# Kernel optimization log

Measured on AMD Instinct MI355X. Metric: run time of the kernel, lower is better.

The kernel has to match this reference:

```python
import jax, jax.numpy as jnp
import numpy as np

N_ENT = 15000
N_REL = 237
HID = 128
N_STEP = 3
EPS = 1e-10
E_BASE = 200000
BATCH, NEG = 8, 16


def _lstm(x, w_ih, w_hh, b_ih, b_hh):
    # x: [T, B, H]; single-layer PyTorch-style LSTM (gate order i, f, g, o)
    B = x.shape[1]
    H = w_hh.shape[1]
    bias = b_ih + b_hh

    def step(carry, xt):
        h, c = carry
        gates = xt @ w_ih.T + h @ w_hh.T + bias  # [B, 4H]
        i, f, g, o = jnp.split(gates, 4, axis=-1)
        c = jax.nn.sigmoid(f) * c + jax.nn.sigmoid(i) * jnp.tanh(g)
        h = jax.nn.sigmoid(o) * jnp.tanh(c)
        return (h, c), h

    init = (jnp.zeros((B, H), x.dtype), jnp.zeros((B, H), x.dtype))
    _, hs = jax.lax.scan(step, init, x)
    return hs  # [T, B, H]


def setup_inputs() -> dict:
    key = jax.random.key(0)
    ks = jax.random.split(key, 16)
    h_index = jax.random.randint(ks[0], (BATCH, NEG), 0, N_ENT)
    t_index = jax.random.randint(ks[1], (BATCH, NEG), 0, N_ENT)
    r_index = jax.random.randint(ks[2], (BATCH, NEG), 0, N_REL)
    src = jax.random.randint(ks[3], (E_BASE,), 0, N_ENT)
    dst = jax.random.randint(ks[4], (E_BASE,), 0, N_ENT)
    rel = jax.random.randint(ks[5], (E_BASE,), 0, N_REL)
    edge_weight = jnp.ones((2 * E_BASE,), jnp.float32)
    s = 0.05
    query_emb = jax.random.normal(ks[6], (2 * N_REL + 1, HID), jnp.float32) * s
    w_ih = jax.random.normal(ks[7], (4 * HID, HID), jnp.float32) * s
    w_hh = jax.random.normal(ks[8], (4 * HID, HID), jnp.float32) * s
    b_ih = jax.random.normal(ks[9], (4 * HID,), jnp.float32) * s
    b_hh = jax.random.normal(ks[10], (4 * HID,), jnp.float32) * s
    weight_w = jax.random.normal(ks[11], (2 * N_REL, HID), jnp.float32) * s
    weight_b = jax.random.normal(ks[12], (2 * N_REL,), jnp.float32) * s
    lin_w = jax.random.normal(ks[13], (), jnp.float32)
    lin_b = jax.random.normal(ks[14], (), jnp.float32)
    return {"query_emb": query_emb, "w_ih": w_ih, "w_hh": w_hh, "b_ih": b_ih,
            "b_hh": b_hh, "weight_w": weight_w, "weight_b": weight_b,
            "lin_w": lin_w, "lin_b": lin_b, "edge_weight": edge_weight,
            "h_index": h_index, "t_index": t_index, "r_index": r_index,
            "src": src, "dst": dst, "rel": rel}


def reference(query_emb, w_ih, w_hh, b_ih, b_hh, weight_w, weight_b,
              lin_w, lin_b, edge_weight, h_index, t_index, r_index,
              src, dst, rel):
    R2 = 2 * N_REL
    # graph.undirected(add_inverse=True): add reversed edges with inverse relations
    node_in = jnp.concatenate([src, dst])
    node_out = jnp.concatenate([dst, src])
    relation = jnp.concatenate([rel, rel + N_REL])

    # negative_sample_to_tail
    is_t_neg = jnp.all(h_index == h_index[:, :1], axis=-1, keepdims=True)
    h_i = jnp.where(is_t_neg, h_index, t_index)
    t_i = jnp.where(is_t_neg, t_index, h_index)
    r_i = jnp.where(is_t_neg, r_index, r_index + N_REL)

    hr = (h_i * R2 + r_i).ravel()
    uniq, inv = jnp.unique(hr, return_inverse=True, size=hr.shape[0], fill_value=0)
    inv = inv.ravel().reshape(h_i.shape)
    h_set = uniq // R2
    r_set = uniq % R2
    B = uniq.shape[0]

    # query sequence: [r]*(T-1) + [end=R2]
    q_idx = jnp.concatenate([jnp.tile(r_set[None], (N_STEP - 1, 1)),
                             jnp.full((1, B), R2, r_set.dtype)], axis=0)
    query = query_emb[q_idx]                      # [T, B, H]
    hidden = _lstm(query, w_ih, w_hh, b_ih, b_hh)  # [T, B, H]

    memory = jax.nn.one_hot(h_set, N_ENT, dtype=query.dtype)[None]  # [1, B, N]
    out = None
    for i in range(N_STEP):
        k = hidden[i]                                   # [B, H]
        attn = jax.nn.softmax(jnp.einsum('bd,tbd->bt', k, hidden[:i + 1]), axis=-1)
        inp = jnp.einsum('bt,tbn->nb', attn, memory)    # [N, B]
        w = jax.nn.softmax(k @ weight_w.T + weight_b, axis=-1).T  # [R2, B]
        # gather -> relation-weight multiply -> scatter_add
        msg = inp[node_in] * w[relation] * edge_weight[:, None]   # [2E, B]
        out = jnp.zeros((N_ENT, B), inp.dtype).at[node_out].add(msg)
        out = out / jnp.maximum(out.sum(axis=0, keepdims=True), EPS)
        memory = jnp.concatenate([memory, out.T[None]], axis=0)

    score = out[t_i, inv]          # [batch, neg]
    return score * lin_w + lin_b
```

## Files before the change

### kernel.cpp

```cpp
#include <hip/hip_runtime.h>
#include <math.h>

#define N_ENT  15000
#define N_RELC 237
#define R2C    474
#define EBASE  200000
#define E2     400000
#define EPSV   1e-10f
#define CAP    72
#define NSLICE 64

typedef unsigned int uint32;
typedef unsigned short ushort16;

__device__ __forceinline__ ushort16 f2bf(float x) {
    uint32 u = __float_as_uint(x);
    u = (u + 0x7FFFu + ((u >> 16) & 1u)) >> 16;
    return (ushort16)u;
}
__device__ __forceinline__ float bflo(uint32 u) { return __uint_as_float(u << 16); }
__device__ __forceinline__ float bfhi(uint32 u) { return __uint_as_float(u & 0xFFFF0000u); }

__global__ void init_kernel(float* __restrict__ out0, int* __restrict__ cursor,
                            float* __restrict__ Swide,
                            const float* __restrict__ w_ih, const float* __restrict__ w_hh,
                            const float* __restrict__ weight_w,
                            float* __restrict__ wit, float* __restrict__ wht,
                            float* __restrict__ wwt,
                            const int* __restrict__ h_index, const int* __restrict__ t_index,
                            const int* __restrict__ r_index,
                            int* __restrict__ h_set, int* __restrict__ r_set,
                            int* __restrict__ invp, int* __restrict__ t_flat,
                            int* __restrict__ headidx) {
    if (blockIdx.x == gridDim.x - 1) {
        __shared__ int sv[128], eq[128], f_[128], uniq[128], hsh[128];
        __shared__ int isneg[8];
        __shared__ int UcntS;
        int j = threadIdx.x;
        for (int idx = j; idx < N_ENT; idx += 256) headidx[idx] = -1;
        __syncthreads();
        int hrv = 0, first = 0, rank = 0;
        if (j < 128) {
            int b = j >> 4;
            int h = h_index[j];
            eq[j] = (h == h_index[b * 16]) ? 1 : 0;
        }
        __syncthreads();
        if (j < 128 && (j & 15) == 0) {
            int b = j >> 4, a = 1;
            for (int q = 0; q < 16; q++) a &= eq[b * 16 + q];
            isneg[b] = a;
        }
        __syncthreads();
        if (j < 128) {
            int b = j >> 4;
            int h = h_index[j], t = t_index[j], r = r_index[j];
            int hi, ti, ri;
            if (isneg[b]) { hi = h; ti = t; ri = r; }
            else          { hi = t; ti = h; ri = r + N_RELC; }
            t_flat[j] = ti;
            hrv = hi * R2C + ri;
            sv[j] = hrv;
            uniq[j] = 0;
        }
        __syncthreads();
        if (j < 128) {
            first = 1;
            for (int q = 0; q < j; q++) if (sv[q] == hrv) { first = 0; break; }
            f_[j] = first;
        }
        __syncthreads();
        if (j < 128) {
            for (int q = 0; q < 128; q++) rank += (f_[q] && sv[q] < hrv) ? 1 : 0;
        }
        if (j == 0) {
            int c = 0;
            for (int q = 0; q < 128; q++) c += f_[q];
            UcntS = c;
        }
        __syncthreads();
        if (j < 128) {
            if (first) uniq[rank] = hrv;
            invp[j] = rank;
        }
        __syncthreads();
        if (j < 128) {
            int uv = uniq[j];
            int hs = uv / R2C;
            h_set[j] = hs;
            r_set[j] = uv % R2C;
            hsh[j] = hs;
        }
        __syncthreads();
        if (j < 128) {
            int U = UcntS;
            int hs = hsh[j];
            if (j < U && (j == 0 || hsh[j - 1] != hs)) {
                int e = j + 1;
                while (e < U && hsh[e] == hs) e++;
                headidx[hs] = (j << 8) | e;
            }
        }
        return;
    }
    int idx = blockIdx.x * 256 + threadIdx.x;
    float4 z4 = make_float4(0.f, 0.f, 0.f, 0.f);
    if (idx < 480000) { ((float4*)out0)[idx] = z4; return; }
    idx -= 480000;
    if (idx < 3750) { ((int4*)cursor)[idx] = make_int4(0, 0, 0, 0); return; }
    idx -= 3750;
    if (idx < 6144) { ((float4*)Swide)[idx] = z4; return; }
    idx -= 6144;
    if (idx < 65536) {
        int d = idx >> 9, g = idx & 511;
        wit[idx] = w_ih[g * 128 + d];
        wht[idx] = w_hh[g * 128 + d];
        return;
    }
    idx -= 65536;
    if (idx < 65536) {
        int d = idx >> 9, r = idx & 511;
        if (r < R2C) wwt[idx] = weight_w[r * 128 + d];
    }
}

__global__ void fill_kernel(const int* __restrict__ src, const int* __restrict__ dst,
                            const int* __restrict__ rel, const float* __restrict__ ew,
                            int* __restrict__ cursor, int2* __restrict__ edata2) {
    int e = blockIdx.x * 256 + threadIdx.x;
    if (e >= E2) return;
    int ni, no, r;
    if (e < EBASE) { ni = src[e]; no = dst[e]; r = rel[e]; }
    else { int e2 = e - EBASE; ni = dst[e2]; no = src[e2]; r = rel[e2] + N_RELC; }
    int pos = atomicAdd(&cursor[no], 1);
    if (pos < CAP)
        edata2[no * CAP + pos] = make_int2((ni << 9) | r, __float_as_int(ew[e]));
}

__global__ void lstm_kernel(const float* __restrict__ query_emb,
                            const int* __restrict__ r_set,
                            const float* __restrict__ wit, const float* __restrict__ wht,
                            const float* __restrict__ b_ih, const float* __restrict__ b_hh,
                            float* __restrict__ hidden) {
    int b = blockIdx.x, g = threadIdx.x;
    __shared__ float x[128], h[128], gl[512];
    float bias = b_ih[g] + b_hh[g];
    if (g < 128) x[g] = query_emb[r_set[b] * 128 + g];
    __syncthreads();
    float p0 = 0.f, p1 = 0.f, p2 = 0.f, p3 = 0.f;
    #pragma unroll 8
    for (int d = 0; d < 128; d += 4) {
        p0 += x[d + 0] * wit[(d + 0) * 512 + g];
        p1 += x[d + 1] * wit[(d + 1) * 512 + g];
        p2 += x[d + 2] * wit[(d + 2) * 512 + g];
        p3 += x[d + 3] * wit[(d + 3) * 512 + g];
    }
    float xpA = bias + ((p0 + p1) + (p2 + p3));
    __syncthreads();
    if (g < 128) x[g] = query_emb[R2C * 128 + g];
    __syncthreads();
    p0 = p1 = p2 = p3 = 0.f;
    #pragma unroll 8
    for (int d = 0; d < 128; d += 4) {
        p0 += x[d + 0] * wit[(d + 0) * 512 + g];
        p1 += x[d + 1] * wit[(d + 1) * 512 + g];
        p2 += x[d + 2] * wit[(d + 2) * 512 + g];
        p3 += x[d + 3] * wit[(d + 3) * 512 + g];
    }
    float xpB = bias + ((p0 + p1) + (p2 + p3));
    if (g < 128) h[g] = 0.f;
    float c = 0.f;
    __syncthreads();
    for (int step = 0; step < 3; step++) {
        float a0 = 0.f, a1 = 0.f, a2 = 0.f, a3 = 0.f;
        #pragma unroll 8
        for (int d = 0; d < 128; d += 4) {
            a0 += h[d + 0] * wht[(d + 0) * 512 + g];
            a1 += h[d + 1] * wht[(d + 1) * 512 + g];
            a2 += h[d + 2] * wht[(d + 2) * 512 + g];
            a3 += h[d + 3] * wht[(d + 3) * 512 + g];
        }
        gl[g] = ((step < 2) ? xpA : xpB) + ((a0 + a1) + (a2 + a3));
        __syncthreads();
        if (g < 128) {
            float ig = gl[g], fg = gl[128 + g], gg = gl[256 + g], og = gl[384 + g];
            float si = 1.f / (1.f + expf(-ig));
            float sf = 1.f / (1.f + expf(-fg));
            float so = 1.f / (1.f + expf(-og));
            c = sf * c + si * tanhf(gg);
            float hh = so * tanhf(c);
            hidden[(step * 128 + b) * 128 + g] = hh;
            h[g] = hh;
        }
        __syncthreads();
    }
}

__global__ void coef_kernel(const float* __restrict__ hidden, int step,
                            const float* __restrict__ Swide,
                            const float* __restrict__ wwt,
                            const float* __restrict__ weight_b,
                            ushort16* __restrict__ wTb, float* __restrict__ attnS) {
    int b = blockIdx.x, tid = threadIdx.x;
    __shared__ float k[128];
    __shared__ float red[256];
    __shared__ float sc[3];
    __shared__ float Ssum[2];
    __shared__ float logit[R2C];
    if (tid < 128) k[tid] = hidden[(step * 128 + b) * 128 + tid];
    __syncthreads();
    for (int t = 0; t <= step; t++) {
        float v = 0.f;
        if (tid < 128) v = k[tid] * hidden[(t * 128 + b) * 128 + tid];
        red[tid] = v;
        __syncthreads();
        for (int s2 = 128; s2 > 0; s2 >>= 1) {
            if (tid < s2) red[tid] += red[tid + s2];
            __syncthreads();
        }
        if (tid == 0) sc[t] = red[0];
        __syncthreads();
    }
    for (int t = 0; t < step; t++) {
        red[tid] = (tid < NSLICE) ? Swide[t * (NSLICE * 128) + tid * 128 + b] : 0.f;
        __syncthreads();
        for (int s2 = 128; s2 > 0; s2 >>= 1) {
            if (tid < s2) red[tid] += red[tid + s2];
            __syncthreads();
        }
        if (tid == 0) Ssum[t] = red[0];
        __syncthreads();
    }
    if (tid == 0) {
        float m = sc[0];
        for (int t2 = 1; t2 <= step; t2++) m = fmaxf(m, sc[t2]);
        float ssum = 0.f;
        float ex[3];
        for (int t2 = 0; t2 <= step; t2++) { ex[t2] = expf(sc[t2] - m); ssum += ex[t2]; }
        for (int t2 = 0; t2 <= step; t2++) {
            float a = ex[t2] / ssum;
            if (t2 > 0) a /= fmaxf(Ssum[t2 - 1], EPSV);
            attnS[b * 4 + t2] = a;
        }
    }
    for (int r = tid; r < R2C; r += 256) {
        float acc = weight_b[r];
        #pragma unroll 8
        for (int d = 0; d < 128; d++) acc += k[d] * wwt[d * 512 + r];
        logit[r] = acc;
    }
    __syncthreads();
    float m = -1e30f;
    for (int r = tid; r < R2C; r += 256) m = fmaxf(m, logit[r]);
    red[tid] = m; __syncthreads();
    for (int s2 = 128; s2 > 0; s2 >>= 1) {
        if (tid < s2) red[tid] = fmaxf(red[tid], red[tid + s2]);
        __syncthreads();
    }
    m = red[0]; __syncthreads();
    float s = 0.f;
    for (int r = tid; r < R2C; r += 256) s += expf(logit[r] - m);
    red[tid] = s; __syncthreads();
    for (int s2 = 128; s2 > 0; s2 >>= 1) {
        if (tid < s2) red[tid] += red[tid + s2];
        __syncthreads();
    }
    float invs = 1.f / red[0];
    for (int r = tid; r < R2C; r += 256)
        wTb[r * 128 + b] = f2bf(expf(logit[r] - m) * invs);
}

__global__ void step0_kernel(const int* __restrict__ src, const int* __restrict__ dst,
                             const int* __restrict__ rel, const float* __restrict__ ew,
                             const int* __restrict__ headidx,
                             const ushort16* __restrict__ wTb,
                             float* __restrict__ out0, float* __restrict__ Sw0) {
    int e = blockIdx.x * 256 + threadIdx.x;
    if (e >= E2) return;
    int ni, no, r;
    if (e < EBASE) { ni = src[e]; no = dst[e]; r = rel[e]; }
    else { int e2 = e - EBASE; ni = dst[e2]; no = src[e2]; r = rel[e2] + N_RELC; }
    int hv = headidx[ni];
    if (hv < 0) return;
    float w = ew[e];
    int b0 = hv >> 8, b1 = hv & 255;
    int sl = (e & (NSLICE - 1)) * 128;
    for (int b = b0; b < b1; b++) {
        float v = __uint_as_float(((uint32)wTb[r * 128 + b]) << 16) * w;
        atomicAdd(&out0[no * 128 + b], v);
        atomicAdd(&Sw0[sl + b], v);
    }
}

__global__ void inp_kernel(const float* __restrict__ o1, const float* __restrict__ o2,
                           int step, const float* __restrict__ attnS,
                           const int* __restrict__ h_set, ushort16* __restrict__ inpb) {
    int b = threadIdx.x;
    float a0 = attnS[b * 4 + 0];
    float a1 = attnS[b * 4 + 1];
    float a2 = (step >= 2) ? attnS[b * 4 + 2] : 0.f;
    int hs = h_set[b];
    for (int n = blockIdx.x; n < N_ENT; n += gridDim.x) {
        float v = (n == hs) ? a0 : 0.f;
        v += a1 * o1[n * 128 + b];
        if (step >= 2) v += a2 * o2[n * 128 + b];
        inpb[n * 128 + b] = f2bf(v);
    }
}

__global__ void gather_kernel(const int2* __restrict__ edata2,
                              const int* __restrict__ cursor,
                              const ushort16* __restrict__ inpb,
                              const ushort16* __restrict__ wTb,
                              float* __restrict__ out, float* __restrict__ Sw) {
    __shared__ float sred[4][128];
    int wid = threadIdx.x >> 6;
    int lane = threadIdx.x & 63;
    int n = blockIdx.x * 4 + wid;
    int deg = cursor[n];
    if (deg > CAP) deg = CAP;
    const int2* ed = edata2 + n * CAP;
    int c2 = lane * 2;
    float ax = 0.f, ay = 0.f;
    int e = 0;
    for (; e + 4 <= deg; e += 4) {
        int2 d0 = ed[e + 0], d1 = ed[e + 1], d2 = ed[e + 2], d3 = ed[e + 3];
        uint32 i0 = *(const uint32*)(inpb + ((d0.x >> 9) << 7) + c2);
        uint32 w0 = *(const uint32*)(wTb  + ((d0.x & 511) << 7) + c2);
        uint32 i1 = *(const uint32*)(inpb + ((d1.x >> 9) << 7) + c2);
        uint32 w1 = *(const uint32*)(wTb  + ((d1.x & 511) << 7) + c2);
        uint32 i2 = *(const uint32*)(inpb + ((d2.x >> 9) << 7) + c2);
        uint32 w2 = *(const uint32*)(wTb  + ((d2.x & 511) << 7) + c2);
        uint32 i3 = *(const uint32*)(inpb + ((d3.x >> 9) << 7) + c2);
        uint32 w3 = *(const uint32*)(wTb  + ((d3.x & 511) << 7) + c2);
        float f0 = __int_as_float(d0.y), f1 = __int_as_float(d1.y);
        float f2 = __int_as_float(d2.y), f3 = __int_as_float(d3.y);
        ax += bflo(i0) * bflo(w0) * f0 + bflo(i1) * bflo(w1) * f1
            + bflo(i2) * bflo(w2) * f2 + bflo(i3) * bflo(w3) * f3;
        ay += bfhi(i0) * bfhi(w0) * f0 + bfhi(i1) * bfhi(w1) * f1
            + bfhi(i2) * bfhi(w2) * f2 + bfhi(i3) * bfhi(w3) * f3;
    }
    for (; e < deg; e++) {
        int2 edv = ed[e];
        float w = __int_as_float(edv.y);
        uint32 ia = *(const uint32*)(inpb + ((edv.x >> 9) << 7) + c2);
        uint32 wa = *(const uint32*)(wTb  + ((edv.x & 511) << 7) + c2);
        ax += bflo(ia) * bflo(wa) * w;
        ay += bfhi(ia) * bfhi(wa) * w;
    }
    *(float2*)(out + n * 128 + c2) = make_float2(ax, ay);
    sred[wid][c2] = ax;
    sred[wid][c2 + 1] = ay;
    __syncthreads();
    if (threadIdx.x < 128) {
        float s = sred[0][threadIdx.x] + sred[1][threadIdx.x]
                + sred[2][threadIdx.x] + sred[3][threadIdx.x];
        atomicAdd(&Sw[(blockIdx.x & (NSLICE - 1)) * 128 + threadIdx.x], s);
    }
}

__global__ void score_kernel(const float* __restrict__ out2, const float* __restrict__ Swide,
                             const int* __restrict__ t_flat, const int* __restrict__ invp,
                             const float* __restrict__ lin_w, const float* __restrict__ lin_b,
                             float* __restrict__ d_out) {
    int j = threadIdx.x;
    int bb = invp[j];
    float s = 0.f;
    for (int s8 = 0; s8 < NSLICE; s8++)
        s += Swide[2 * (NSLICE * 128) + s8 * 128 + bb];
    d_out[j] = out2[t_flat[j] * 128 + bb] / fmaxf(s, EPSV) * lin_w[0] + lin_b[0];
}

extern "C" void kernel_launch(void* const* d_in, const int* in_sizes, int n_in,
                              void* d_out, int out_size, void* d_ws, size_t ws_size,
                              hipStream_t stream) {
    const float* query_emb  = (const float*)d_in[0];
    const float* w_ih       = (const float*)d_in[1];
    const float* w_hh       = (const float*)d_in[2];
    const float* b_ih       = (const float*)d_in[3];
    const float* b_hh       = (const float*)d_in[4];
    const float* weight_w   = (const float*)d_in[5];
    const float* weight_b   = (const float*)d_in[6];
    const float* lin_w      = (const float*)d_in[7];
    const float* lin_b      = (const float*)d_in[8];
    const float* edge_weight= (const float*)d_in[9];
    const int*   h_index    = (const int*)d_in[10];
    const int*   t_index    = (const int*)d_in[11];
    const int*   r_index    = (const int*)d_in[12];
    const int*   src        = (const int*)d_in[13];
    const int*   dst        = (const int*)d_in[14];
    const int*   rel        = (const int*)d_in[15];
    float* out = (float*)d_out;

    char* ws = (char*)d_ws;
    size_t off_b = 0;
    auto alloc = [&](size_t bytes) -> void* {
        void* p = ws + off_b;
        off_b = (off_b + bytes + 255) & ~(size_t)255;
        return p;
    };
    float*    hidden  = (float*)alloc(3 * 128 * 128 * sizeof(float));
    float*    attnS   = (float*)alloc(128 * 4 * sizeof(float));
    ushort16* wTb     = (ushort16*)alloc(R2C * 128 * sizeof(ushort16));
    float*    Swide   = (float*)alloc(3 * NSLICE * 128 * sizeof(float));
    float*    wit     = (float*)alloc(512 * 128 * sizeof(float));
    float*    wht     = (float*)alloc(512 * 128 * sizeof(float));
    float*    wwt     = (float*)alloc(512 * 128 * sizeof(float));
    int*      h_set   = (int*)alloc(128 * sizeof(int));
    int*      r_set   = (int*)alloc(128 * sizeof(int));
    int*      invp    = (int*)alloc(128 * sizeof(int));
    int*      t_flat  = (int*)alloc(128 * sizeof(int));
    int*      cursor  = (int*)alloc(N_ENT * sizeof(int));
    int*      headidx = (int*)alloc(N_ENT * sizeof(int));
    int2*     edata2  = (int2*)alloc((size_t)N_ENT * CAP * sizeof(int2));
    ushort16* inpb    = (ushort16*)alloc((size_t)N_ENT * 128 * sizeof(ushort16));
    float*    outs0   = (float*)alloc((size_t)N_ENT * 128 * sizeof(float));
    float*    outs1   = (float*)alloc((size_t)N_ENT * 128 * sizeof(float));

    init_kernel<<<2427, 256, 0, stream>>>(outs0, cursor, Swide, w_ih, w_hh, weight_w,
                                          wit, wht, wwt, h_index, t_index, r_index,
                                          h_set, r_set, invp, t_flat, headidx);
    fill_kernel<<<(E2 + 255) / 256, 256, 0, stream>>>(src, dst, rel, edge_weight,
                                                      cursor, edata2);
    lstm_kernel<<<128, 512, 0, stream>>>(query_emb, r_set, wit, wht, b_ih, b_hh, hidden);

    coef_kernel<<<128, 256, 0, stream>>>(hidden, 0, Swide, wwt, weight_b, wTb, attnS);
    step0_kernel<<<(E2 + 255) / 256, 256, 0, stream>>>(src, dst, rel, edge_weight,
                                                       headidx, wTb, outs0, Swide);

    coef_kernel<<<128, 256, 0, stream>>>(hidden, 1, Swide, wwt, weight_b, wTb, attnS);
    inp_kernel<<<2048, 128, 0, stream>>>(outs0, outs1, 1, attnS, h_set, inpb);
    gather_kernel<<<N_ENT / 4, 256, 0, stream>>>(edata2, cursor, inpb, wTb,
                                                 outs1, Swide + NSLICE * 128);

    coef_kernel<<<128, 256, 0, stream>>>(hidden, 2, Swide, wwt, weight_b, wTb, attnS);
    inp_kernel<<<2048, 128, 0, stream>>>(outs0, outs1, 2, attnS, h_set, inpb);
    gather_kernel<<<N_ENT / 4, 256, 0, stream>>>(edata2, cursor, inpb, wTb,
                                                 outs0, Swide + 2 * NSLICE * 128);

    score_kernel<<<1, 128, 0, stream>>>(outs0, Swide, t_flat, invp, lin_w, lin_b, out);
}
```

Before: 166.9 us.

## Fuse LSTM with edge fill, compact step0 hits, bf16 out1, fold score into gather

Merges the LSTM and CSR fill kernels into one launch and has the fill pass also build a compacted list of edges whose source is a head entity. Step 0 then processes only that short list instead of rescanning all 400k edges. The intermediate step-1 output is stored in bf16 to halve its traffic, and the gather is reworked so each half-wave reads 4 columns over alternating edges. The final score computation moves into the last block of the step-2 gather using a done counter. This removes several launches and redundant passes, at the cost of an extra atomic per hit, a fixed hit-list capacity, and extra bf16 rounding.

```diff
diff --git a/kernel.cpp b/kernel.cpp
--- a/kernel.cpp
+++ b/kernel.cpp
@@ -9,6 +9,7 @@
 #define EPSV   1e-10f
 #define CAP    72
 #define NSLICE 64
+#define HITCAP 65536
 
 typedef unsigned int uint32;
 typedef unsigned short ushort16;
@@ -20,9 +21,12 @@
 }
 __device__ __forceinline__ float bflo(uint32 u) { return __uint_as_float(u << 16); }
 __device__ __forceinline__ float bfhi(uint32 u) { return __uint_as_float(u & 0xFFFF0000u); }
+__device__ __forceinline__ uint32 pk2(float lo, float hi) {
+    return (uint32)f2bf(lo) | ((uint32)f2bf(hi) << 16);
+}
 
 __global__ void init_kernel(float* __restrict__ out0, int* __restrict__ cursor,
-                            float* __restrict__ Swide,
+                            float* __restrict__ Swide, int* __restrict__ misc,
                             const float* __restrict__ w_ih, const float* __restrict__ w_hh,
                             const float* __restrict__ weight_w,
                             float* __restrict__ wit, float* __restrict__ wht,
@@ -42,8 +46,7 @@
         int hrv = 0, first = 0, rank = 0;
         if (j < 128) {
             int b = j >> 4;
-            int h = h_index[j];
-            eq[j] = (h == h_index[b * 16]) ? 1 : 0;
+            eq[j] = (h_index[j] == h_index[b * 16]) ? 1 : 0;
         }
         __syncthreads();
         if (j < 128 && (j & 15) == 0) {
@@ -86,10 +89,9 @@
         __syncthreads();
         if (j < 128) {
             int uv = uniq[j];
-            int hs = uv / R2C;
-            h_set[j] = hs;
+            h_set[j] = uv / R2C;
             r_set[j] = uv % R2C;
-            hsh[j] = hs;
+            hsh[j] = uv / R2C;
         }
         __syncthreads();
         if (j < 128) {
@@ -111,6 +113,8 @@
     idx -= 3750;
     if (idx < 6144) { ((float4*)Swide)[idx] = z4; return; }
     idx -= 6144;
+    if (idx < 2) { ((int4*)misc)[idx] = make_int4(0, 0, 0, 0); return; }
+    idx -= 2;
     if (idx < 65536) {
         int d = idx >> 9, g = idx & 511;
         wit[idx] = w_ih[g * 128 + d];
@@ -124,75 +128,84 @@
     }
 }
 
-__global__ void fill_kernel(const int* __restrict__ src, const int* __restrict__ dst,
-                            const int* __restrict__ rel, const float* __restrict__ ew,
-                            int* __restrict__ cursor, int2* __restrict__ edata2) {
-    int e = blockIdx.x * 256 + threadIdx.x;
+__global__ void build_kernel(const float* __restrict__ query_emb,
+                             const int* __restrict__ r_set,
+                             const float* __restrict__ wit, const float* __restrict__ wht,
+                             const float* __restrict__ b_ih, const float* __restrict__ b_hh,
+                             float* __restrict__ hidden,
+                             const int* __restrict__ src, const int* __restrict__ dst,
+                             const int* __restrict__ rel, const float* __restrict__ ew,
+                             const int* __restrict__ headidx,
+                             int* __restrict__ cursor, int2* __restrict__ edata2,
+                             int* __restrict__ hitcnt, int4* __restrict__ hitlist) {
+    if (blockIdx.x < 128) {
+        int b = blockIdx.x, g = threadIdx.x;
+        __shared__ float x[128], h[128], gl[512];
+        float bias = b_ih[g] + b_hh[g];
+        if (g < 128) x[g] = query_emb[r_set[b] * 128 + g];
+        __syncthreads();
+        float p0 = 0.f, p1 = 0.f, p2 = 0.f, p3 = 0.f;
+        #pragma unroll 8
+        for (int d = 0; d < 128; d += 4) {
+            p0 += x[d + 0] * wit[(d + 0) * 512 + g];
+            p1 += x[d + 1] * wit[(d + 1) * 512 + g];
+            p2 += x[d + 2] * wit[(d + 2) * 512 + g];
+            p3 += x[d + 3] * wit[(d + 3) * 512 + g];
+        }
+        float xpA = bias + ((p0 + p1) + (p2 + p3));
+        __syncthreads();
+        if (g < 128) x[g] = query_emb[R2C * 128 + g];
+        __syncthreads();
+        p0 = p1 = p2 = p3 = 0.f;
+        #pragma unroll 8
+        for (int d = 0; d < 128; d += 4) {
+            p0 += x[d + 0] * wit[(d + 0) * 512 + g];
+            p1 += x[d + 1] * wit[(d + 1) * 512 + g];
+            p2 += x[d + 2] * wit[(d + 2) * 512 + g];
+            p3 += x[d + 3] * wit[(d + 3) * 512 + g];
+        }
+        float xpB = bias + ((p0 + p1) + (p2 + p3));
+        if (g < 128) h[g] = 0.f;
+        float c = 0.f;
+        __syncthreads();
+        for (int step = 0; step < 3; step++) {
+            float a0 = 0.f, a1 = 0.f, a2 = 0.f, a3 = 0.f;
+            #pragma unroll 8
+            for (int d = 0; d < 128; d += 4) {
+                a0 += h[d + 0] * wht[(d + 0) * 512 + g];
+                a1 += h[d + 1] * wht[(d + 1) * 512 + g];
+                a2 += h[d + 2] * wht[(d + 2) * 512 + g];
+                a3 += h[d + 3] * wht[(d + 3) * 512 + g];
+            }
+            gl[g] = ((step < 2) ? xpA : xpB) + ((a0 + a1) + (a2 + a3));
+            __syncthreads();
+            if (g < 128) {
+                float ig = gl[g], fg = gl[128 + g], gg = gl[256 + g], og = gl[384 + g];
+                float si = 1.f / (1.f + expf(-ig));
+                float sf = 1.f / (1.f + expf(-fg));
+                float so = 1.f / (1.f + expf(-og));
+                c = sf * c + si * tanhf(gg);
+                float hh = so * tanhf(c);
+                hidden[(step * 128 + b) * 128 + g] = hh;
+                h[g] = hh;
+            }
+            __syncthreads();
+        }
+        return;
+    }
+    int e = (blockIdx.x - 128) * 512 + threadIdx.x;
     if (e >= E2) return;
     int ni, no, r;
     if (e < EBASE) { ni = src[e]; no = dst[e]; r = rel[e]; }
     else { int e2 = e - EBASE; ni = dst[e2]; no = src[e2]; r = rel[e2] + N_RELC; }
+    float w = ew[e];
     int pos = atomicAdd(&cursor[no], 1);
     if (pos < CAP)
-        edata2[no * CAP + pos] = make_int2((ni << 9) | r, __float_as_int(ew[e]));
-}
-
-__global__ void lstm_kernel(const float* __restrict__ query_emb,
-                            const int* __restrict__ r_set,
-                            const float* __restrict__ wit, const float* __restrict__ wht,
-                            const float* __restrict__ b_ih, const float* __restrict__ b_hh,
-                            float* __restrict__ hidden) {
-    int b = blockIdx.x, g = threadIdx.x;
-    __shared__ float x[128], h[128], gl[512];
-    float bias = b_ih[g] + b_hh[g];
-    if (g < 128) x[g] = query_emb[r_set[b] * 128 + g];
-    __syncthreads();
-    float p0 = 0.f, p1 = 0.f, p2 = 0.f, p3 = 0.f;
-    #pragma unroll 8
-    for (int d = 0; d < 128; d += 4) {
-        p0 += x[d + 0] * wit[(d + 0) * 512 + g];
-        p1 += x[d + 1] * wit[(d + 1) * 512 + g];
-        p2 += x[d + 2] * wit[(d + 2) * 512 + g];
-        p3 += x[d + 3] * wit[(d + 3) * 512 + g];
-    }
-    float xpA = bias + ((p0 + p1) + (p2 + p3));
-    __syncthreads();
-    if (g < 128) x[g] = query_emb[R2C * 128 + g];
-    __syncthreads();
-    p0 = p1 = p2 = p3 = 0.f;
-    #pragma unroll 8
-    for (int d = 0; d < 128; d += 4) {
-        p0 += x[d + 0] * wit[(d + 0) * 512 + g];
-        p1 += x[d + 1] * wit[(d + 1) * 512 + g];
-        p2 += x[d + 2] * wit[(d + 2) * 512 + g];
-        p3 += x[d + 3] * wit[(d + 3) * 512 + g];
-    }
-    float xpB = bias + ((p0 + p1) + (p2 + p3));
-    if (g < 128) h[g] = 0.f;
-    float c = 0.f;
-    __syncthreads();
-    for (int step = 0; step < 3; step++) {
-        float a0 = 0.f, a1 = 0.f, a2 = 0.f, a3 = 0.f;
-        #pragma unroll 8
-        for (int d = 0; d < 128; d += 4) {
-            a0 += h[d + 0] * wht[(d + 0) * 512 + g];
-            a1 += h[d + 1] * wht[(d + 1) * 512 + g];
-            a2 += h[d + 2] * wht[(d + 2) * 512 + g];
-            a3 += h[d + 3] * wht[(d + 3) * 512 + g];
-        }
-        gl[g] = ((step < 2) ? xpA : xpB) + ((a0 + a1) + (a2 + a3));
-        __syncthreads();
-        if (g < 128) {
-            float ig = gl[g], fg = gl[128 + g], gg = gl[256 + g], og = gl[384 + g];
-            float si = 1.f / (1.f + expf(-ig));
-            float sf = 1.f / (1.f + expf(-fg));
-            float so = 1.f / (1.f + expf(-og));
-            c = sf * c + si * tanhf(gg);
-            float hh = so * tanhf(c);
-            hidden[(step * 128 + b) * 128 + g] = hh;
-            h[g] = hh;
-        }
-        __syncthreads();
+        edata2[no * CAP + pos] = make_int2((ni << 9) | r, __float_as_int(w));
+    int hv = headidx[ni];
+    if (hv >= 0) {
+        int p = atomicAdd(hitcnt, 1);
+        if (p < HITCAP) hitlist[p] = make_int4(no, r, hv, __float_as_int(w));
     }
 }
 
@@ -270,21 +283,18 @@
         wTb[r * 128 + b] = f2bf(expf(logit[r] - m) * invs);
 }
 
-__global__ void step0_kernel(const int* __restrict__ src, const int* __restrict__ dst,
-                             const int* __restrict__ rel, const float* __restrict__ ew,
-                             const int* __restrict__ headidx,
+__global__ void step0_kernel(const int4* __restrict__ hitlist,
+                             const int* __restrict__ hitcnt,
                              const ushort16* __restrict__ wTb,
                              float* __restrict__ out0, float* __restrict__ Sw0) {
-    int e = blockIdx.x * 256 + threadIdx.x;
-    if (e >= E2) return;
-    int ni, no, r;
-    if (e < EBASE) { ni = src[e]; no = dst[e]; r = rel[e]; }
-    else { int e2 = e - EBASE; ni = dst[e2]; no = src[e2]; r = rel[e2] + N_RELC; }
-    int hv = headidx[ni];
-    if (hv < 0) return;
-    float w = ew[e];
-    int b0 = hv >> 8, b1 = hv & 255;
-    int sl = (e & (NSLICE - 1)) * 128;
+    int idx = blockIdx.x * 256 + threadIdx.x;
+    int cnt = *hitcnt;
+    if (cnt > HITCAP) cnt = HITCAP;
+    if (idx >= cnt) return;
+    int4 hv = hitlist[idx];
+    int no = hv.x, r = hv.y, b0 = hv.z >> 8, b1 = hv.z & 255;
+    float w = __int_as_float(hv.w);
+    int sl = (idx & (NSLICE - 1)) * 128;
     for (int b = b0; b < b1; b++) {
         float v = __uint_as_float(((uint32)wTb[r * 128 + b]) << 16) * w;
         atomicAdd(&out0[no * 128 + b], v);
@@ -292,7 +302,7 @@
     }
 }
 
-__global__ void inp_kernel(const float* __restrict__ o1, const float* __restrict__ o2,
+__global__ void inp_kernel(const float* __restrict__ o1, const ushort16* __restrict__ o2b,
                            int step, const float* __restrict__ attnS,
                            const int* __restrict__ h_set, ushort16* __restrict__ inpb) {
     int b = threadIdx.x;
@@ -303,72 +313,91 @@
     for (int n = blockIdx.x; n < N_ENT; n += gridDim.x) {
         float v = (n == hs) ? a0 : 0.f;
         v += a1 * o1[n * 128 + b];
-        if (step >= 2) v += a2 * o2[n * 128 + b];
+        if (step >= 2) v += a2 * __uint_as_float(((uint32)o2b[n * 128 + b]) << 16);
         inpb[n * 128 + b] = f2bf(v);
     }
 }
 
+template<int MODE>
 __global__ void gather_kernel(const int2* __restrict__ edata2,
                               const int* __restrict__ cursor,
                               const ushort16* __restrict__ inpb,
                               const ushort16* __restrict__ wTb,
-                              float* __restrict__ out, float* __restrict__ Sw) {
+                              float* __restrict__ outf, ushort16* __restrict__ outb,
+                              float* __restrict__ Sw, int* __restrict__ done,
+                              const int* __restrict__ t_flat, const int* __restrict__ invp,
+                              const float* __restrict__ lin_w, const float* __restrict__ lin_b,
+                              float* __restrict__ d_out) {
     __shared__ float sred[4][128];
+    __shared__ int lastf;
     int wid = threadIdx.x >> 6;
     int lane = threadIdx.x & 63;
     int n = blockIdx.x * 4 + wid;
     int deg = cursor[n];
     if (deg > CAP) deg = CAP;
     const int2* ed = edata2 + n * CAP;
-    int c2 = lane * 2;
-    float ax = 0.f, ay = 0.f;
-    int e = 0;
-    for (; e + 4 <= deg; e += 4) {
-        int2 d0 = ed[e + 0], d1 = ed[e + 1], d2 = ed[e + 2], d3 = ed[e + 3];
-        uint32 i0 = *(const uint32*)(inpb + ((d0.x >> 9) << 7) + c2);
-        uint32 w0 = *(const uint32*)(wTb  + ((d0.x & 511) << 7) + c2);
-        uint32 i1 = *(const uint32*)(inpb + ((d1.x >> 9) << 7) + c2);
-        uint32 w1 = *(const uint32*)(wTb  + ((d1.x & 511) << 7) + c2);
-        uint32 i2 = *(const uint32*)(inpb + ((d2.x >> 9) << 7) + c2);
-        uint32 w2 = *(const uint32*)(wTb  + ((d2.x & 511) << 7) + c2);
-        uint32 i3 = *(const uint32*)(inpb + ((d3.x >> 9) << 7) + c2);
-        uint32 w3 = *(const uint32*)(wTb  + ((d3.x & 511) << 7) + c2);
-        float f0 = __int_as_float(d0.y), f1 = __int_as_float(d1.y);
-        float f2 = __int_as_float(d2.y), f3 = __int_as_float(d3.y);
-        ax += bflo(i0) * bflo(w0) * f0 + bflo(i1) * bflo(w1) * f1
-            + bflo(i2) * bflo(w2) * f2 + bflo(i3) * bflo(w3) * f3;
-        ay += bfhi(i0) * bfhi(w0) * f0 + bfhi(i1) * bfhi(w1) * f1
-            + bfhi(i2) * bfhi(w2) * f2 + bfhi(i3) * bfhi(w3) * f3;
-    }
-    for (; e < deg; e++) {
-        int2 edv = ed[e];
-        float w = __int_as_float(edv.y);
-        uint32 ia = *(const uint32*)(inpb + ((edv.x >> 9) << 7) + c2);
-        uint32 wa = *(const uint32*)(wTb  + ((edv.x & 511) << 7) + c2);
-        ax += bflo(ia) * bflo(wa) * w;
-        ay += bfhi(ia) * bfhi(wa) * w;
-    }
-    *(float2*)(out + n * 128 + c2) = make_float2(ax, ay);
-    sred[wid][c2] = ax;
-    sred[wid][c2 + 1] = ay;
+    int half = lane >> 5;
+    int c4 = (lane & 31) << 2;
+    float a0 = 0.f, a1 = 0.f, a2 = 0.f, a3 = 0.f;
+    int e = half;
+    for (; e + 2 < deg; e += 4) {
+        int2 dA = ed[e], dB = ed[e + 2];
+        uint2 ivA = *(const uint2*)(inpb + ((dA.x >> 9) << 7) + c4);
+        uint2 wvA = *(const uint2*)(wTb  + ((dA.x & 511) << 7) + c4);
+        uint2 ivB = *(const uint2*)(inpb + ((dB.x >> 9) << 7) + c4);
+        uint2 wvB = *(const uint2*)(wTb  + ((dB.x & 511) << 7) + c4);
+        float wA = __int_as_float(dA.y), wB = __int_as_float(dB.y);
+        a0 += bflo(ivA.x) * bflo(wvA.x) * wA + bflo(ivB.x) * bflo(wvB.x) * wB;
+        a1 += bfhi(ivA.x) * bfhi(wvA.x) * wA + bfhi(ivB.x) * bfhi(wvB.x) * wB;
+        a2 += bflo(ivA.y) * bflo(wvA.y) * wA + bflo(ivB.y) * bflo(wvB.y) * wB;
+        a3 += bfhi(ivA.y) * bfhi(wvA.y) * wA + bfhi(ivB.y) * bfhi(wvB.y) * wB;
+    }
+    if (e < deg) {
+        int2 dA = ed[e];
+        uint2 ivA = *(const uint2*)(inpb + ((dA.x >> 9) << 7) + c4);
+        uint2 wvA = *(const uint2*)(wTb  + ((dA.x & 511) << 7) + c4);
+        float wA = __int_as_float(dA.y);
+        a0 += bflo(ivA.x) * bflo(wvA.x) * wA;
+        a1 += bfhi(ivA.x) * bfhi(wvA.x) * wA;
+        a2 += bflo(ivA.y) * bflo(wvA.y) * wA;
+        a3 += bfhi(ivA.y) * bfhi(wvA.y) * wA;
+    }
+    a0 += __shfl_xor(a0, 32);
+    a1 += __shfl_xor(a1, 32);
+    a2 += __shfl_xor(a2, 32);
+    a3 += __shfl_xor(a3, 32);
+    if (half == 0) {
+        if (MODE == 0) {
+            *(uint2*)((ushort16*)outb + (n << 7) + c4) = make_uint2(pk2(a0, a1), pk2(a2, a3));
+        } else {
+            *(float4*)(outf + n * 128 + c4) = make_float4(a0, a1, a2, a3);
+        }
+        sred[wid][c4 + 0] = a0;
+        sred[wid][c4 + 1] = a1;
+        sred[wid][c4 + 2] = a2;
+        sred[wid][c4 + 3] = a3;
+    }
     __syncthreads();
     if (threadIdx.x < 128) {
         float s = sred[0][threadIdx.x] + sred[1][threadIdx.x]
                 + sred[2][threadIdx.x] + sred[3][threadIdx.x];
         atomicAdd(&Sw[(blockIdx.x & (NSLICE - 1)) * 128 + threadIdx.x], s);
     }
-}
-
-__global__ void score_kernel(const float* __restrict__ out2, const float* __restrict__ Swide,
-                             const int* __restrict__ t_flat, const int* __restrict__ invp,
-                             const float* __restrict__ lin_w, const float* __restrict__ lin_b,
-                             float* __restrict__ d_out) {
-    int j = threadIdx.x;
-    int bb = invp[j];
-    float s = 0.f;
-    for (int s8 = 0; s8 < NSLICE; s8++)
-        s += Swide[2 * (NSLICE * 128) + s8 * 128 + bb];
-    d_out[j] = out2[t_flat[j] * 128 + bb] / fmaxf(s, EPSV) * lin_w[0] + lin_b[0];
+    if (MODE == 1) {
+        __threadfence();
+        if (threadIdx.x == 0)
+            lastf = (atomicAdd(done, 1) == (int)gridDim.x - 1);
+        __syncthreads();
+        if (lastf) {
+            __threadfence();
+            if (threadIdx.x < 128) {
+                int j = threadIdx.x, bb = invp[j];
+                float s = 0.f;
+                for (int sl = 0; sl < NSLICE; sl++) s += Sw[sl * 128 + bb];
+                d_out[j] = outf[t_flat[j] * 128 + bb] / fmaxf(s, EPSV) * lin_w[0] + lin_b[0];
+            }
+        }
+    }
 }
 
 extern "C" void kernel_launch(void* const* d_in, const int* in_sizes, int n_in,
@@ -412,31 +441,35 @@
     int*      t_flat  = (int*)alloc(128 * sizeof(int));
     int*      cursor  = (int*)alloc(N_ENT * sizeof(int));
     int*      headidx = (int*)alloc(N_ENT * sizeof(int));
+    int*      misc    = (int*)alloc(8 * sizeof(int));
     int2*     edata2  = (int2*)alloc((size_t)N_ENT * CAP * sizeof(int2));
     ushort16* inpb    = (ushort16*)alloc((size_t)N_ENT * 128 * sizeof(ushort16));
     float*    outs0   = (float*)alloc((size_t)N_ENT * 128 * sizeof(float));
-    float*    outs1   = (float*)alloc((size_t)N_ENT * 128 * sizeof(float));
-
-    init_kernel<<<2427, 256, 0, stream>>>(outs0, cursor, Swide, w_ih, w_hh, weight_w,
-                                          wit, wht, wwt, h_index, t_index, r_index,
+    ushort16* out1b   = (ushort16*)alloc((size_t)N_ENT * 128 * sizeof(ushort16));
+    int4*     hitlist = (int4*)alloc((size_t)HITCAP * sizeof(int4));
+    int* hitcnt = misc;
+    int* done   = misc + 1;
+
+    init_kernel<<<2427, 256, 0, stream>>>(outs0, cursor, Swide, misc,
+                                          w_ih, w_hh, weight_w, wit, wht, wwt,
+                                          h_index, t_index, r_index,
                                           h_set, r_set, invp, t_flat, headidx);
-    fill_kernel<<<(E2 + 255) / 256, 256, 0, stream>>>(src, dst, rel, edge_weight,
-                                                      cursor, edata2);
-    lstm_kernel<<<128, 512, 0, stream>>>(query_emb, r_set, wit, wht, b_ih, b_hh, hidden);
+    build_kernel<<<128 + (E2 + 511) / 512, 512, 0, stream>>>(
+        query_emb, r_set, wit, wht, b_ih, b_hh, hidden,
+        src, dst, rel, edge_weight, headidx, cursor, edata2, hitcnt, hitlist);
 
     coef_kernel<<<128, 256, 0, stream>>>(hidden, 0, Swide, wwt, weight_b, wTb, attnS);
-    step0_kernel<<<(E2 + 255) / 256, 256, 0, stream>>>(src, dst, rel, edge_weight,
-                                                       headidx, wTb, outs0, Swide);
+    step0_kernel<<<HITCAP / 256, 256, 0, stream>>>(hitlist, hitcnt, wTb, outs0, Swide);
 
     coef_kernel<<<128, 256, 0, stream>>>(hidden, 1, Swide, wwt, weight_b, wTb, attnS);
-    inp_kernel<<<2048, 128, 0, stream>>>(outs0, outs1, 1, attnS, h_set, inpb);
-    gather_kernel<<<N_ENT / 4, 256, 0, stream>>>(edata2, cursor, inpb, wTb,
-                                                 outs1, Swide + NSLICE * 128);
+    inp_kernel<<<2048, 128, 0, stream>>>(outs0, out1b, 1, attnS, h_set, inpb);
+    gather_kernel<0><<<N_ENT / 4, 256, 0, stream>>>(edata2, cursor, inpb, wTb,
+                                                    nullptr, out1b, Swide + NSLICE * 128,
+                                                    done, t_flat, invp, lin_w, lin_b, out);
 
     coef_kernel<<<128, 256, 0, stream>>>(hidden, 2, Swide, wwt, weight_b, wTb, attnS);
-    inp_kernel<<<2048, 128, 0, stream>>>(outs0, outs1, 2, attnS, h_set, inpb);
-    gather_kernel<<<N_ENT / 4, 256, 0, stream>>>(edata2, cursor, inpb, wTb,
-                                                 outs0, Swide + 2 * NSLICE * 128);
-
-    score_kernel<<<1, 128, 0, stream>>>(outs0, Swide, t_flat, invp, lin_w, lin_b, out);
-}
+    inp_kernel<<<2048, 128, 0, stream>>>(outs0, out1b, 2, attnS, h_set, inpb);
+    gather_kernel<1><<<N_ENT / 4, 256, 0, stream>>>(edata2, cursor, inpb, wTb,
+                                                    outs0, nullptr, Swide + 2 * NSLICE * 128,
+                                                    done, t_flat, invp, lin_w, lin_b, out);
+}
```

New measurement: 453.8 us. +171.9%, slower.
